# Optimization experiments

Hardware: AMD Instinct MI355X
Metric: run time of the kernel (lower is better)

Reference implementation:

```python
import jax, jax.numpy as jnp
import numpy as np
from jax import lax

B, T, IN, H, OUT = 4096, 512, 2, 12, 2


def setup_inputs() -> dict:
    key = jax.random.key(0)
    ks = jax.random.split(key, 11)
    s = 1.0 / np.sqrt(H)  # PyTorch LSTM init scale
    f32 = jnp.float32
    return {
        "x": jax.random.normal(ks[0], (B, T, IN), dtype=f32),
        "W_ih0": jax.random.uniform(ks[1], (4 * H, IN), dtype=f32, minval=-s, maxval=s),
        "W_hh0": jax.random.uniform(ks[2], (4 * H, H), dtype=f32, minval=-s, maxval=s),
        "b_ih0": jax.random.uniform(ks[3], (4 * H,), dtype=f32, minval=-s, maxval=s),
        "b_hh0": jax.random.uniform(ks[4], (4 * H,), dtype=f32, minval=-s, maxval=s),
        "W_ih1": jax.random.uniform(ks[5], (4 * H, H), dtype=f32, minval=-s, maxval=s),
        "W_hh1": jax.random.uniform(ks[6], (4 * H, H), dtype=f32, minval=-s, maxval=s),
        "b_ih1": jax.random.uniform(ks[7], (4 * H,), dtype=f32, minval=-s, maxval=s),
        "b_hh1": jax.random.uniform(ks[8], (4 * H,), dtype=f32, minval=-s, maxval=s),
        "fc_W": jax.random.uniform(ks[9], (OUT, H), dtype=f32, minval=-s, maxval=s),
        "fc_b": jax.random.uniform(ks[10], (OUT,), dtype=f32, minval=-s, maxval=s),
    }


def _lstm_layer(x, W_ih, W_hh, b_ih, b_hh):
    # x: [B, T, in_dim] -> hidden trajectory [B, T, H]
    b, h = x.shape[0], W_hh.shape[1]
    # Precompute input contribution for all timesteps: [T, B, 4H]
    xg = jnp.einsum('bti,gi->tbg', x, W_ih) + b_ih + b_hh

    def step(carry, xg_t):
        hprev, cprev = carry
        gates = xg_t + hprev @ W_hh.T  # [B, 4H], PyTorch gate order i,f,g,o
        i, f, g, o = jnp.split(gates, 4, axis=-1)
        i = jax.nn.sigmoid(i)
        f = jax.nn.sigmoid(f)
        g = jnp.tanh(g)
        o = jax.nn.sigmoid(o)
        c = f * cprev + i * g
        hnew = o * jnp.tanh(c)
        return (hnew, c), hnew

    z = jnp.zeros((b, h), dtype=x.dtype)
    _, hs = lax.scan(step, (z, z), xg)  # hs: [T, B, H]
    return jnp.swapaxes(hs, 0, 1)  # [B, T, H]


def reference(x, W_ih0, W_hh0, b_ih0, b_hh0, W_ih1, W_hh1, b_ih1, b_hh1, fc_W, fc_b):
    # 2-layer LSTM, h0=c0=0; dropout is identity in eval mode.
    h1 = _lstm_layer(x, W_ih0, W_hh0, b_ih0, b_hh0)   # [B, T, H]
    h2 = _lstm_layer(h1, W_ih1, W_hh1, b_ih1, b_hh1)  # [B, T, H]
    last = h2[:, -1, :]                               # [B, H]
    return last @ fc_W.T + fc_b                       # [B, OUT]
```

## Files before the change

### kernel.cpp

```cpp
#include <hip/hip_runtime.h>


namespace {
constexpr int H  = 12;
constexpr int T  = 512;
constexpr float LOG2E = 1.4426950408889634f;

typedef float f2 __attribute__((ext_vector_type(2)));

__device__ __forceinline__ f2 fma2(f2 a, f2 b, f2 c) {
    return __builtin_elementwise_fma(a, b, c);
}
__device__ __forceinline__ float exp2_(float x) {
    float r; asm("v_exp_f32 %0, %1" : "=v"(r) : "v"(x)); return r;
}
__device__ __forceinline__ float rcp_(float x) { return __builtin_amdgcn_rcpf(x); }
__device__ __forceinline__ void memfence_() { asm volatile("" ::: "memory"); }

template <int CTRL>
__device__ __forceinline__ float dppf(float v) {
    return __int_as_float(__builtin_amdgcn_update_dpp(
        __float_as_int(v), __float_as_int(v), CTRL, 0xF, 0xF, true));
}
constexpr int BC0 = 0x00;
constexpr int BC1 = 0x55;
constexpr int BC2 = 0xAA;
constexpr int BC3 = 0xFF;

__device__ __forceinline__ float tanh_(float c) {
    return fmaf(2.0f, rcp_(1.0f + exp2_(-2.0f * LOG2E * c)), -1.0f);
}
}

__global__ __launch_bounds__(256, 4) void lstm2_fc_kernel(
    const float* __restrict__ x,
    const float* __restrict__ W_ih0,
    const float* __restrict__ W_hh0,
    const float* __restrict__ b_ih0,
    const float* __restrict__ b_hh0,
    const float* __restrict__ W_ih1,
    const float* __restrict__ W_hh1,
    const float* __restrict__ b_ih1,
    const float* __restrict__ b_hh1,
    const float* __restrict__ fc_W,
    const float* __restrict__ fc_b,
    float* __restrict__ out)
{
    const int lane = threadIdx.x & 63;
    const int wid  = __builtin_amdgcn_readfirstlane((int)threadIdx.x >> 6);
    const int b    = blockIdx.x * 4 + wid;
    const int u    = lane >> 2;
    const int gate = lane & 3;
    const int uc   = (u < H) ? u : 0;
    const int r    = gate * H + uc;

    const float pre  = (gate == 2) ? 2.0f : 1.0f;
    const float kmul = -LOG2E * pre;
    const float pa   = 1.0f - pre;

    __shared__ __align__(16) float sm[4 * 32];
    float* smb = &sm[wid * 32];
    const bool isL1 = (gate == 1);
    const bool pub  = (gate <= 1) && (u < H);
    float* smw = smb + (isL1 ? 16 : 0) + uc;

    f2 wx, whh0p[6], wih1p[6], whh1p[6];
    wx.x = kmul * W_ih0[r * 2 + 0];
    wx.y = kmul * W_ih0[r * 2 + 1];
#pragma unroll
    for (int k = 0; k < 6; ++k) {
        whh0p[k].x = kmul * W_hh0[r * H + 2 * k];
        whh0p[k].y = kmul * W_hh0[r * H + 2 * k + 1];
        wih1p[k].x = kmul * W_ih1[r * H + 2 * k];
        wih1p[k].y = kmul * W_ih1[r * H + 2 * k + 1];
        whh1p[k].x = kmul * W_hh1[r * H + 2 * k];
        whh1p[k].y = kmul * W_hh1[r * H + 2 * k + 1];
    }
    f2 bias0p, bias1p;
    bias0p.x = kmul * (b_ih0[r] + b_hh0[r]); bias0p.y = 0.0f;
    bias1p.x = kmul * (b_ih1[r] + b_hh1[r]); bias1p.y = 0.0f;

    float c = 0.0f;
    float I1s = 0.0f, F1s = 0.0f, G1s = 0.0f, O1s = 0.0f;
    f2 hp0[6], hq1[6];
#pragma unroll
    for (int k = 0; k < 6; ++k) { hp0[k] = (f2)(0.0f); hq1[k] = (f2)(0.0f); }

    const float* xp = x + (size_t)b * T * 2;

    auto step = [&](float xv0, float xv1) {
        f2 xv; xv.x = xv0; xv.y = xv1;
        f2 cA = fma2(wx, xv, bias0p);
        cA = fma2(whh0p[0], hp0[0], cA);
        cA = fma2(whh0p[1], hp0[1], cA);
        f2 cB = whh0p[2] * hp0[2];
        cB = fma2(whh0p[3], hp0[3], cB);
        f2 cC = whh0p[4] * hp0[4];
        cC = fma2(whh0p[5], hp0[5], cC);
        cA = cA + cB + cC;
        const float s0 = fmaf(pre, rcp_(1.0f + exp2_(cA.x + cA.y)), pa);
        const float I0 = dppf<BC0>(s0);
        const float F0 = dppf<BC1>(s0);
        const float G0 = dppf<BC2>(s0);
        const float O0 = dppf<BC3>(s0);
        const float I = isL1 ? I1s : I0;
        const float F = isL1 ? F1s : F0;
        const float G = isL1 ? G1s : G0;
        const float O = isL1 ? O1s : O0;
        c = fmaf(F, c, I * G);
        const float hv = O * tanh_(c);
        if (pub) *smw = hv;
        memfence_();
#pragma unroll
        for (int k = 0; k < 6; ++k) hp0[k] = *(const f2*)(smb + 2 * k);
#pragma unroll
        for (int k = 0; k < 6; ++k) hq1[k] = *(const f2*)(smb + 16 + 2 * k);
        f2 dA = fma2(whh1p[0], hq1[0], bias1p);
        dA = fma2(wih1p[0], hp0[0], dA);
        dA = fma2(whh1p[1], hq1[1], dA);
        dA = fma2(wih1p[1], hp0[1], dA);
        f2 dB = whh1p[2] * hq1[2];
        dB = fma2(wih1p[2], hp0[2], dB);
        dB = fma2(whh1p[3], hq1[3], dB);
        dB = fma2(wih1p[3], hp0[3], dB);
        f2 dC = whh1p[4] * hq1[4];
        dC = fma2(wih1p[4], hp0[4], dC);
        dC = fma2(whh1p[5], hq1[5], dC);
        dC = fma2(wih1p[5], hp0[5], dC);
        dA = dA + dB + dC;
        const float s1 = fmaf(pre, rcp_(1.0f + exp2_(dA.x + dA.y)), pa);
        I1s = dppf<BC0>(s1);
        F1s = dppf<BC1>(s1);
        G1s = dppf<BC2>(s1);
        O1s = dppf<BC3>(s1);
    };

    float2 xc = *(const float2*)xp;
    for (int t = 0; t < T - 1; ++t) {
        const float2 xn = *(const float2*)(xp + 2 * (t + 1));
        step(xc.x, xc.y);
        xc = xn;
    }
    step(xc.x, xc.y);

    {
        const float cE = fmaf(F1s, c, I1s * G1s);
        const float hE = O1s * tanh_(cE);
        if (pub && isL1) *smw = hE;
        memfence_();
    }

    if (lane == 0) {
        float r0 = fc_b[0];
        float r1 = fc_b[1];
#pragma unroll
        for (int j = 0; j < H; ++j) {
            const float hj = smb[16 + j];
            r0 = fmaf(fc_W[j],     hj, r0);
            r1 = fmaf(fc_W[H + j], hj, r1);
        }
        float2 res; res.x = r0; res.y = r1;
        *(float2*)(out + (size_t)b * 2) = res;
    }
}

extern "C" void kernel_launch(void* const* d_in, const int* in_sizes, int n_in,
                              void* d_out, int out_size, void* d_ws, size_t ws_size,
                              hipStream_t stream) {
    const float* x     = (const float*)d_in[0];
    const float* W_ih0 = (const float*)d_in[1];
    const float* W_hh0 = (const float*)d_in[2];
    const float* b_ih0 = (const float*)d_in[3];
    const float* b_hh0 = (const float*)d_in[4];
    const float* W_ih1 = (const float*)d_in[5];
    const float* W_hh1 = (const float*)d_in[6];
    const float* b_ih1 = (const float*)d_in[7];
    const float* b_hh1 = (const float*)d_in[8];
    const float* fc_W  = (const float*)d_in[9];
    const float* fc_b  = (const float*)d_in[10];
    float* out = (float*)d_out;

    lstm2_fc_kernel<<<1024, 256, 0, stream>>>(
        x, W_ih0, W_hh0, b_ih0, b_hh0,
        W_ih1, W_hh1, b_ih1, b_hh1, fc_W, fc_b, out);
}
```

Baseline: 252.8 us.

## Restructure LSTM wavefront pipeline to compute both layer cell updates per step

Changes the two-layer skewed pipeline so that lane gate==0 owns both cell states c0 and c1 and computes both layer updates within each step, instead of splitting the cell update between gate 0 and gate 1 lanes using values carried from the previous step. This removes the select logic and the I0 DPP broadcast, and peels the first and last steps explicitly. The trade-off is a longer serial chain per step (layer-1 activation and cell update now happen inside the same step before the shared-memory exchange) and the removal of the 16-byte alignment on the shared buffer used for f2 loads.

```diff
diff --git a/kernel.cpp b/kernel.cpp
--- a/kernel.cpp
+++ b/kernel.cpp
@@ -2,8 +2,8 @@
 
 
 namespace {
-constexpr int H  = 12;
-constexpr int T  = 512;
+constexpr int H = 12;
+constexpr int T = 512;
 constexpr float LOG2E = 1.4426950408889634f;
 
 typedef float f2 __attribute__((ext_vector_type(2)));
@@ -22,7 +22,6 @@
     return __int_as_float(__builtin_amdgcn_update_dpp(
         __float_as_int(v), __float_as_int(v), CTRL, 0xF, 0xF, true));
 }
-constexpr int BC0 = 0x00;
 constexpr int BC1 = 0x55;
 constexpr int BC2 = 0xAA;
 constexpr int BC3 = 0xFF;
@@ -58,11 +57,11 @@
     const float kmul = -LOG2E * pre;
     const float pa   = 1.0f - pre;
 
-    __shared__ __align__(16) float sm[4 * 32];
+    __shared__ float sm[4 * 32];
     float* smb = &sm[wid * 32];
-    const bool isL1 = (gate == 1);
-    const bool pub  = (gate <= 1) && (u < H);
-    float* smw = smb + (isL1 ? 16 : 0) + uc;
+    const bool writer = (gate == 0) && (u < H);
+    float* smw0 = smb + uc;
+    float* smw1 = smb + 16 + uc;
 
     f2 wx, whh0p[6], wih1p[6], whh1p[6];
     wx.x = kmul * W_ih0[r * 2 + 0];
@@ -80,16 +79,39 @@
     bias0p.x = kmul * (b_ih0[r] + b_hh0[r]); bias0p.y = 0.0f;
     bias1p.x = kmul * (b_ih1[r] + b_hh1[r]); bias1p.y = 0.0f;
 
-    float c = 0.0f;
-    float I1s = 0.0f, F1s = 0.0f, G1s = 0.0f, O1s = 0.0f;
+    float c0 = 0.0f, c1 = 0.0f;
     f2 hp0[6], hq1[6];
 #pragma unroll
     for (int k = 0; k < 6; ++k) { hp0[k] = (f2)(0.0f); hq1[k] = (f2)(0.0f); }
 
     const float* xp = x + (size_t)b * T * 2;
-
-    auto step = [&](float xv0, float xv1) {
-        f2 xv; xv.x = xv0; xv.y = xv1;
+    float2 xc = *(const float2*)xp;
+
+    {
+        f2 xv; xv.x = xc.x; xv.y = xc.y;
+        f2 cA = fma2(wx, xv, bias0p);
+        const float s0 = fmaf(pre, rcp_(1.0f + exp2_(cA.x + cA.y)), pa);
+        const float F0 = dppf<BC1>(s0);
+        const float G0 = dppf<BC2>(s0);
+        const float O0 = dppf<BC3>(s0);
+        (void)F0;
+        c0 = s0 * G0;
+        const float h0v = O0 * tanh_(c0);
+        if (writer) { *smw0 = h0v; *smw1 = 0.0f; }
+        memfence_();
+#pragma unroll
+        for (int k = 0; k < 6; ++k) hp0[k] = *(const f2*)(smb + 2 * k);
+#pragma unroll
+        for (int k = 0; k < 6; ++k) hq1[k] = *(const f2*)(smb + 16 + 2 * k);
+        memfence_();
+        xc = *(const float2*)(xp + 2);
+    }
+
+    for (int t = 1; t < T; ++t) {
+        const int tn = (t < T - 1) ? (t + 1) : t;
+        const float2 xn = *(const float2*)(xp + 2 * tn);
+
+        f2 xv; xv.x = xc.x; xv.y = xc.y;
         f2 cA = fma2(wx, xv, bias0p);
         cA = fma2(whh0p[0], hp0[0], cA);
         cA = fma2(whh0p[1], hp0[1], cA);
@@ -99,22 +121,13 @@
         cC = fma2(whh0p[5], hp0[5], cC);
         cA = cA + cB + cC;
         const float s0 = fmaf(pre, rcp_(1.0f + exp2_(cA.x + cA.y)), pa);
-        const float I0 = dppf<BC0>(s0);
         const float F0 = dppf<BC1>(s0);
         const float G0 = dppf<BC2>(s0);
         const float O0 = dppf<BC3>(s0);
-        const float I = isL1 ? I1s : I0;
-        const float F = isL1 ? F1s : F0;
-        const float G = isL1 ? G1s : G0;
-        const float O = isL1 ? O1s : O0;
-        c = fmaf(F, c, I * G);
-        const float hv = O * tanh_(c);
-        if (pub) *smw = hv;
-        memfence_();
-#pragma unroll
-        for (int k = 0; k < 6; ++k) hp0[k] = *(const f2*)(smb + 2 * k);
-#pragma unroll
-        for (int k = 0; k < 6; ++k) hq1[k] = *(const f2*)(smb + 16 + 2 * k);
+        c0 = fmaf(F0, c0, s0 * G0);
+        const float h0v = O0 * tanh_(c0);
+        if (writer) *smw0 = h0v;
+
         f2 dA = fma2(whh1p[0], hq1[0], bias1p);
         dA = fma2(wih1p[0], hp0[0], dA);
         dA = fma2(whh1p[1], hq1[1], dA);
@@ -129,35 +142,57 @@
         dC = fma2(wih1p[5], hp0[5], dC);
         dA = dA + dB + dC;
         const float s1 = fmaf(pre, rcp_(1.0f + exp2_(dA.x + dA.y)), pa);
-        I1s = dppf<BC0>(s1);
-        F1s = dppf<BC1>(s1);
-        G1s = dppf<BC2>(s1);
-        O1s = dppf<BC3>(s1);
-    };
-
-    float2 xc = *(const float2*)xp;
-    for (int t = 0; t < T - 1; ++t) {
-        const float2 xn = *(const float2*)(xp + 2 * (t + 1));
-        step(xc.x, xc.y);
+        const float F1 = dppf<BC1>(s1);
+        const float G1 = dppf<BC2>(s1);
+        const float O1 = dppf<BC3>(s1);
+        c1 = fmaf(F1, c1, s1 * G1);
+        const float h1v = O1 * tanh_(c1);
+        if (writer) *smw1 = h1v;
+
+        memfence_();
+#pragma unroll
+        for (int k = 0; k < 6; ++k) hp0[k] = *(const f2*)(smb + 2 * k);
+#pragma unroll
+        for (int k = 0; k < 6; ++k) hq1[k] = *(const f2*)(smb + 16 + 2 * k);
+        memfence_();
         xc = xn;
     }
-    step(xc.x, xc.y);
 
     {
-        const float cE = fmaf(F1s, c, I1s * G1s);
-        const float hE = O1s * tanh_(cE);
-        if (pub && isL1) *smw = hE;
-        memfence_();
+        f2 dA = fma2(whh1p[0], hq1[0], bias1p);
+        dA = fma2(wih1p[0], hp0[0], dA);
+        dA = fma2(whh1p[1], hq1[1], dA);
+        dA = fma2(wih1p[1], hp0[1], dA);
+        f2 dB = whh1p[2] * hq1[2];
+        dB = fma2(wih1p[2], hp0[2], dB);
+        dB = fma2(whh1p[3], hq1[3], dB);
+        dB = fma2(wih1p[3], hp0[3], dB);
+        f2 dC = whh1p[4] * hq1[4];
+        dC = fma2(wih1p[4], hp0[4], dC);
+        dC = fma2(whh1p[5], hq1[5], dC);
+        dC = fma2(wih1p[5], hp0[5], dC);
+        dA = dA + dB + dC;
+        const float s1 = fmaf(pre, rcp_(1.0f + exp2_(dA.x + dA.y)), pa);
+        const float F1 = dppf<BC1>(s1);
+        const float G1 = dppf<BC2>(s1);
+        const float O1 = dppf<BC3>(s1);
+        c1 = fmaf(F1, c1, s1 * G1);
+        const float h1v = O1 * tanh_(c1);
+        if (writer) *smw1 = h1v;
+        memfence_();
+#pragma unroll
+        for (int k = 0; k < 6; ++k) hq1[k] = *(const f2*)(smb + 16 + 2 * k);
     }
 
     if (lane == 0) {
         float r0 = fc_b[0];
         float r1 = fc_b[1];
 #pragma unroll
-        for (int j = 0; j < H; ++j) {
-            const float hj = smb[16 + j];
-            r0 = fmaf(fc_W[j],     hj, r0);
-            r1 = fmaf(fc_W[H + j], hj, r1);
+        for (int k = 0; k < 6; ++k) {
+            r0 = fmaf(fc_W[2 * k],     hq1[k].x, r0);
+            r0 = fmaf(fc_W[2 * k + 1], hq1[k].y, r0);
+            r1 = fmaf(fc_W[H + 2 * k],     hq1[k].x, r1);
+            r1 = fmaf(fc_W[H + 2 * k + 1], hq1[k].y, r1);
         }
         float2 res; res.x = r0; res.y = r1;
         *(float2*)(out + (size_t)b * 2) = res;
```

Measured after the change: 261.9 us. +3.6%, slower.
